# Performance work log

Hardware: AMD Instinct MI355X
Metric: run time of the kernel (lower is better)

The kernel has to match this reference:

```python
import jax, jax.numpy as jnp
import numpy as np

D = 512; H = 8; DH = 64; DI = H * DH   # dim, heads, dim_head, attn inner dim
L = 6                                   # num_blocks
NEX = 6                                 # num_message_exchanges
FFI = int(D * 4.0 * 2 / 3)              # 1365, GEGLU inner dim
V = 32000                               # num_tokens (vocab)
B, N = 2, 192                           # batch, seq_len
EPS = 1.1920929e-07                     # torch nn.RMSNorm default eps (fp32 finfo eps)


def rmsnorm(x, w):
    return x * jax.lax.rsqrt(jnp.mean(x * x, axis=-1, keepdims=True) + EPS) * w


def _heads(t):
    return t.reshape(t.shape[:-1] + (H, DH))


def _block_attn(x, nw, qw, kvw, ow):
    # x: [L, b, n, D]; per-block weights have leading L (vmap over blocks)
    h = rmsnorm(x, nw[:, None, None, :])
    q = _heads(jnp.einsum('lbnd,led->lbne', h, qw))
    kv = jnp.einsum('lbnd,lfd->lbnf', h, kvw)
    k, v = map(_heads, jnp.split(kv, 2, axis=-1))
    sim = jnp.einsum('lbihd,lbjhd->lbhij', q, k)  # NOTE: original never applies 1/sqrt(d) scale
    attn = jax.nn.softmax(sim, axis=-1)
    o = jnp.einsum('lbhij,lbjhd->lbihd', attn, v)
    o = o.reshape(o.shape[:-2] + (DI,))
    return jnp.einsum('lbne,lde->lbnd', o, ow)


def _block_ff(x, nw, kw, kb, vw, vb):
    h = rmsnorm(x, nw[:, None, None, :])
    z = jnp.einsum('lbnd,lfd->lbnf', h, kw) + kb[:, None, None, :]
    sim, gates = jnp.split(z, 2, axis=-1)
    act = sim * jax.nn.gelu(gates, approximate=False)
    return jnp.einsum('lbnf,ldf->lbnd', act, vw) + vb[:, None, None, :]


def _pooled_attn(q_in, ctx, nw, knw, qw, kvw, ow):
    # single-query cross attention; q_in: [B', n, D], ctx: [B', n, M, D]
    qn = rmsnorm(q_in, nw)
    cn = rmsnorm(ctx, nw)
    q = _heads(jnp.einsum('bnd,ed->bne', qn, qw))
    kv = jnp.einsum('bnmd,fd->bnmf', cn, kvw)
    k, v = map(_heads, jnp.split(kv, 2, axis=-1))
    k = rmsnorm(k, knw)  # key_rmsnorm=True on residual/message attention
    sim = jnp.einsum('bnhd,bnmhd->bnhm', q, k)  # unscaled, faithful
    attn = jax.nn.softmax(sim, axis=-1)
    o = jnp.einsum('bnhm,bnmhd->bnhd', attn, v).reshape(q_in.shape[:-1] + (DI,))
    return jnp.einsum('bne,de->bnd', o, ow)


def _forward(tokens, attn_norm_w, attn_q_w, attn_kv_w, attn_out_w,
             ff_norm_w, ff_keys_w, ff_keys_b, ff_vals_w, ff_vals_b,
             res_norm_w, res_keynorm_w, res_q_w, res_kv_w, res_out_w,
             query_readout, ro_norm_w, ro_w):
    b, n, _ = tokens.shape
    toks = jnp.broadcast_to(tokens[None], (L, b, n, D))
    messages = [toks]
    for i in range(NEX):
        attended = _block_attn(toks, attn_norm_w, attn_q_w, attn_kv_w, attn_out_w)
        mem = _block_ff(toks, ff_norm_w, ff_keys_w, ff_keys_b, ff_vals_w, ff_vals_b)
        messages += [attended, mem]
        if i == NEX - 1:
            continue
        packed = jnp.concatenate(messages, axis=0)  # [M, b, n, D], M = len(messages)*L
        M = packed.shape[0]
        # repeat 'm b n d -> (b l) n m d' : all messages broadcast to every block
        am = jnp.broadcast_to(jnp.transpose(packed, (1, 2, 0, 3))[:, None],
                              (b, L, n, M, D)).reshape(b * L, n, M, D)
        # queries flattened (l b)-major vs context (b l)-major -- faithful to original pairing
        qs = toks.reshape(L * b, n, D)
        pooled = _pooled_attn(qs, am, res_norm_w, res_keynorm_w, res_q_w, res_kv_w, res_out_w)
        toks = pooled.reshape(L, b, n, D)
    # rearrange messages 'm l b n d -> b n (m l) d'
    all_m = jnp.transpose(jnp.stack(messages), (2, 3, 0, 1, 4)).reshape(b, n, -1, D)
    qr = jnp.broadcast_to(query_readout, (b, n, D))
    ro = _pooled_attn(qr, all_m, res_norm_w, res_keynorm_w, res_q_w, res_kv_w, res_out_w)
    return jnp.einsum('bnd,vd->bnv', rmsnorm(ro, ro_norm_w), ro_w)


def setup_inputs() -> dict:
    key = jax.random.key(0)
    ks = jax.random.split(key, 16)
    s = 0.02
    def rn(k, shape):
        return jax.random.normal(k, shape, jnp.float32) * s
    return {
        'tokens': jax.random.normal(ks[0], (B, N, D), jnp.float32),
        'attn_norm_w': jnp.ones((L, D), jnp.float32),
        'attn_q_w': rn(ks[1], (L, DI, D)),
        'attn_kv_w': rn(ks[2], (L, 2 * DI, D)),
        'attn_out_w': rn(ks[3], (L, D, DI)),
        'ff_norm_w': jnp.ones((L, D), jnp.float32),
        'ff_keys_w': rn(ks[4], (L, 2 * FFI, D)),
        'ff_keys_b': rn(ks[5], (L, 2 * FFI)),
        'ff_vals_w': rn(ks[6], (L, D, FFI)),
        'ff_vals_b': rn(ks[7], (L, D)),
        'res_norm_w': jnp.ones((D,), jnp.float32),
        'res_keynorm_w': jnp.ones((DH,), jnp.float32),
        'res_q_w': rn(ks[8], (DI, D)),
        'res_kv_w': rn(ks[9], (2 * DI, D)),
        'res_out_w': rn(ks[10], (D, DI)),
        'query_readout': rn(ks[11], (D,)) * 0.5,  # randn * 0.01 as in original init
        'ro_norm_w': jnp.ones((D,), jnp.float32),
        'ro_w': rn(ks[12], (V, D)),
    }


def reference(tokens, attn_norm_w, attn_q_w, attn_kv_w, attn_out_w,
              ff_norm_w, ff_keys_w, ff_keys_b, ff_vals_w, ff_vals_b,
              res_norm_w, res_keynorm_w, res_q_w, res_kv_w, res_out_w,
              query_readout, ro_norm_w, ro_w):
    return _forward(tokens, attn_norm_w, attn_q_w, attn_kv_w, attn_out_w,
                    ff_norm_w, ff_keys_w, ff_keys_b, ff_vals_w, ff_vals_b,
                    res_norm_w, res_keynorm_w, res_q_w, res_kv_w, res_out_w,
                    query_readout, ro_norm_w, ro_w)
```

## Files before the change

### kernel.cpp

```cpp
#include <hip/hip_runtime.h>
#include <hip/hip_bf16.h>
#include <math.h>


#define EPSV 1.1920929e-07f
typedef __hip_bfloat16 bf16;
typedef __attribute__((ext_vector_type(4))) float f32x4;
typedef __attribute__((ext_vector_type(8))) short bf16x8;

__device__ inline void split8r(f32x4 x0, f32x4 x1, bf16x8& h8, bf16x8& l8) {
#pragma unroll
  for (int i = 0; i < 4; ++i) {
    bf16 h0 = __float2bfloat16(x0[i]);
    h8[i] = __builtin_bit_cast(short, h0);
    l8[i] = __builtin_bit_cast(short, __float2bfloat16(x0[i] - __bfloat162float(h0)));
    bf16 h1 = __float2bfloat16(x1[i]);
    h8[i + 4] = __builtin_bit_cast(short, h1);
    l8[i + 4] = __builtin_bit_cast(short, __float2bfloat16(x1[i] - __bfloat162float(h1)));
  }
}

#define BKG 32
#define LDB 40
template <int BMN, int MR>
__global__ __launch_bounds__(256) void gemm_split_t(
    const float* __restrict__ A, const float* __restrict__ W,
    const float* __restrict__ bias, float* __restrict__ C,
    int M, int N, int K, int ldc,
    long long aStr, long long wStr, long long bStr, long long cStr, int mode)
{
  int batch = blockIdx.z;
  A += (size_t)batch * aStr;
  W += (size_t)batch * wStr;
  C += (size_t)batch * cStr;
  if (bias) bias += (size_t)batch * bStr;
  int m0 = blockIdx.y * BMN, n0 = blockIdx.x * BMN;

  __shared__ short Ah[BMN * LDB], Al[BMN * LDB];
  __shared__ short Wh[BMN * LDB], Wl[BMN * LDB];

  int t = threadIdx.x;
  int wave = t >> 6, lane = t & 63;
  const int HALF = BMN / 2;
  const int NR = BMN / 64;
  int wr = wave >> 1, wc = wave & 1;
  int fr = lane & 15, fq = lane >> 4;
  int srow = t >> 2;
  int scol = (t & 3) * 8;

  f32x4 acc[MR][MR] = {};
  f32x4 pa0[NR], pa1[NR], pw0[NR], pw1[NR];

#pragma unroll
  for (int r = 0; r < NR; ++r) {
    int row = r * 64 + srow;
    const float* pa = A + (size_t)(m0 + row) * K + scol;
    const float* pw = W + (size_t)(n0 + row) * K + scol;
    pa0[r] = *(const f32x4*)pa;  pa1[r] = *(const f32x4*)(pa + 4);
    pw0[r] = *(const f32x4*)pw;  pw1[r] = *(const f32x4*)(pw + 4);
  }

  for (int k0 = 0; k0 < K; k0 += BKG) {
#pragma unroll
    for (int r = 0; r < NR; ++r) {
      int row = r * 64 + srow;
      bf16x8 h, l;
      split8r(pa0[r], pa1[r], h, l);
      *(bf16x8*)&Ah[row * LDB + scol] = h;
      *(bf16x8*)&Al[row * LDB + scol] = l;
      split8r(pw0[r], pw1[r], h, l);
      *(bf16x8*)&Wh[row * LDB + scol] = h;
      *(bf16x8*)&Wl[row * LDB + scol] = l;
    }
    if (k0 + BKG < K) {
      int kn = k0 + BKG;
#pragma unroll
      for (int r = 0; r < NR; ++r) {
        int row = r * 64 + srow;
        const float* pa = A + (size_t)(m0 + row) * K + kn + scol;
        const float* pw = W + (size_t)(n0 + row) * K + kn + scol;
        pa0[r] = *(const f32x4*)pa;  pa1[r] = *(const f32x4*)(pa + 4);
        pw0[r] = *(const f32x4*)pw;  pw1[r] = *(const f32x4*)(pw + 4);
      }
    }
    __syncthreads();
    bf16x8 ah[MR], al[MR], wh[MR], wl[MR];
#pragma unroll
    for (int m = 0; m < MR; ++m) {
      int r = (wr * HALF + m * 16 + fr) * LDB + fq * 8;
      ah[m] = *(const bf16x8*)&Ah[r];
      al[m] = *(const bf16x8*)&Al[r];
    }
#pragma unroll
    for (int n = 0; n < MR; ++n) {
      int r = (wc * HALF + n * 16 + fr) * LDB + fq * 8;
      wh[n] = *(const bf16x8*)&Wh[r];
      wl[n] = *(const bf16x8*)&Wl[r];
    }
#pragma unroll
    for (int m = 0; m < MR; ++m)
#pragma unroll
      for (int n = 0; n < MR; ++n) {
        acc[m][n] = __builtin_amdgcn_mfma_f32_16x16x32_bf16(ah[m], wh[n], acc[m][n], 0, 0, 0);
        acc[m][n] = __builtin_amdgcn_mfma_f32_16x16x32_bf16(al[m], wh[n], acc[m][n], 0, 0, 0);
        acc[m][n] = __builtin_amdgcn_mfma_f32_16x16x32_bf16(ah[m], wl[n], acc[m][n], 0, 0, 0);
      }
    __syncthreads();
  }

  if (mode == 0) {
#pragma unroll
    for (int m = 0; m < MR; ++m)
#pragma unroll
      for (int n = 0; n < MR; ++n) {
        int col = n0 + wc * HALF + n * 16 + fr;
        if (col >= N) continue;
        float bv = bias ? bias[col] : 0.f;
#pragma unroll
        for (int j = 0; j < 4; ++j) {
          int row = m0 + wr * HALF + m * 16 + fq * 4 + j;
          if (row < M) C[(size_t)row * ldc + col] = acc[m][n][j] + bv;
        }
      }
  } else {
#pragma unroll
    for (int m = 0; m < MR; ++m)
#pragma unroll
      for (int n = 0; n < MR; ++n) {
        int col = n0 + wc * HALF + n * 16 + fr;
        float bv = bias[col];
#pragma unroll
        for (int j = 0; j < 4; ++j) {
          float z = acc[m][n][j] + bv;
          float zn = __shfl_xor(z, 1);
          if (!(col & 1) && col < N) {
            float g = zn;
            float a = z * (0.5f * g * (1.f + erff(g * 0.70710678118654752f)));
            int row = m0 + wr * HALF + m * 16 + fq * 4 + j;
            if (row < M) C[(size_t)row * ldc + (col >> 1)] = a;
          }
        }
      }
  }
}

__global__ void ffk_perm_kernel(const float* __restrict__ kw,
                                const float* __restrict__ kb,
                                float* __restrict__ wout, float* __restrict__ bout)
{
  size_t idx = (size_t)blockIdx.x * 256 + threadIdx.x;
  const size_t per = 2816ull * 512;
  if (idx < 6 * per) {
    int b = (int)(idx / per);
    size_t r2 = idx % per;
    int r = (int)(r2 >> 9), k = (int)(r2 & 511);
    float v = 0.f;
    if (r < 2730) {
      int c = (r >> 1) + (r & 1) * 1365;
      v = kw[((size_t)b * 2730 + c) * 512 + k];
    }
    wout[idx] = v;
  }
  if (idx < 6 * 2816) {
    int b = (int)(idx / 2816), r = (int)(idx % 2816);
    float v = 0.f;
    if (r < 2730) {
      int c = (r >> 1) + (r & 1) * 1365;
      v = kb[(size_t)b * 2730 + c];
    }
    bout[idx] = v;
  }
}

__global__ void ffv_pad_kernel(const float* __restrict__ vw, float* __restrict__ wout)
{
  size_t idx = (size_t)blockIdx.x * 256 + threadIdx.x;
  const size_t total = 6ull * 512 * 1408;
  if (idx >= total) return;
  int k = (int)(idx % 1408);
  size_t nr = idx / 1408;
  wout[idx] = (k < 1365) ? vw[nr * 1365 + k] : 0.f;
}

__global__ __launch_bounds__(256) void rmsnorm_kernel(
    const float* __restrict__ x, const float* __restrict__ w,
    float* __restrict__ out, int rows_per_w)
{
  int r = blockIdx.x;
  int t = threadIdx.x;
  const float* xr = x + (size_t)r * 512;
  float a = xr[t], b = xr[t + 256];
  float ss = a * a + b * b;
  for (int off = 32; off; off >>= 1) ss += __shfl_xor(ss, off);
  __shared__ float wsum[4];
  if ((t & 63) == 0) wsum[t >> 6] = ss;
  __syncthreads();
  float tot = wsum[0] + wsum[1] + wsum[2] + wsum[3];
  float rs = rsqrtf(tot * (1.f / 512.f) + EPSV);
  const float* wr = w + (size_t)(r / rows_per_w) * 512;
  out[(size_t)r * 512 + t] = a * rs * wr[t];
  out[(size_t)r * 512 + t + 256] = b * rs * wr[t + 256];
}

__global__ __launch_bounds__(256) void rmsnorm2_kernel(
    const float* __restrict__ x, const float* __restrict__ w1,
    const float* __restrict__ w2, float* __restrict__ o1,
    float* __restrict__ o2, int rows_per_w)
{
  int r = blockIdx.x;
  int t = threadIdx.x;
  const float* xr = x + (size_t)r * 512;
  float a = xr[t], b = xr[t + 256];
  float ss = a * a + b * b;
  for (int off = 32; off; off >>= 1) ss += __shfl_xor(ss, off);
  __shared__ float wsum[4];
  if ((t & 63) == 0) wsum[t >> 6] = ss;
  __syncthreads();
  float tot = wsum[0] + wsum[1] + wsum[2] + wsum[3];
  float rs = rsqrtf(tot * (1.f / 512.f) + EPSV);
  int wrow = r / rows_per_w;
  float ar = a * rs, br = b * rs;
  o1[(size_t)r * 512 + t]       = ar * w1[(size_t)wrow * 512 + t];
  o1[(size_t)r * 512 + t + 256] = br * w1[(size_t)wrow * 512 + t + 256];
  o2[(size_t)r * 512 + t]       = ar * w2[(size_t)wrow * 512 + t];
  o2[(size_t)r * 512 + t + 256] = br * w2[(size_t)wrow * 512 + t + 256];
}

__global__ void bcast_kernel(const float* __restrict__ tokens, float* __restrict__ toks)
{
  size_t idx = (size_t)blockIdx.x * 256 + threadIdx.x;
  const size_t total = (size_t)6 * 2 * 192 * 512;
  if (idx >= total) return;
  toks[idx] = tokens[idx % ((size_t)2 * 192 * 512)];
}

__global__ __launch_bounds__(512) void block_attn_kernel(
    const float* __restrict__ q, const float* __restrict__ kv, float* __restrict__ o)
{
  int h = blockIdx.y, lb = blockIdx.z;
  int t = threadIdx.x;
  int wave = t >> 6, lane = t & 63;
  int i = blockIdx.x * 8 + wave;

  __shared__ float Ks[192][65];
  __shared__ float qs[8][64];
  __shared__ float ps[8][192];

  const float* kb = kv + (size_t)lb * 192 * 1024 + h * 64;
#pragma unroll
  for (int c = 0; c < 24; ++c) {
    int idx = c * 512 + t;
    int row = idx >> 6, col = idx & 63;
    Ks[row][col] = kb[(size_t)row * 1024 + col];
  }
  const float* qrow = q + ((size_t)(lb * 192 + i)) * 512 + h * 64;
  qs[wave][lane] = qrow[lane];
  __syncthreads();

  float s[3];
#pragma unroll
  for (int r = 0; r < 3; ++r) {
    int j = lane + r * 64;
    float acc = 0.f;
#pragma unroll 8
    for (int d = 0; d < 64; ++d) acc += qs[wave][d] * Ks[j][d];
    s[r] = acc;
  }
  float mx = fmaxf(fmaxf(s[0], s[1]), s[2]);
  for (int off = 32; off; off >>= 1) mx = fmaxf(mx, __shfl_xor(mx, off));
  float sum = 0.f;
#pragma unroll
  for (int r = 0; r < 3; ++r) { s[r] = expf(s[r] - mx); sum += s[r]; }
  for (int off = 32; off; off >>= 1) sum += __shfl_xor(sum, off);
  float inv = 1.f / sum;
#pragma unroll
  for (int r = 0; r < 3; ++r) ps[wave][lane + r * 64] = s[r] * inv;

  __syncthreads();
  const float* vb = kb + 512;
#pragma unroll
  for (int c = 0; c < 24; ++c) {
    int idx = c * 512 + t;
    int row = idx >> 6, col = idx & 63;
    Ks[row][col] = vb[(size_t)row * 1024 + col];
  }
  __syncthreads();
  float acc = 0.f;
  for (int j = 0; j < 192; ++j) acc += ps[wave][j] * Ks[j][lane];
  o[((size_t)(lb * 192 + i)) * 512 + h * 64 + lane] = acc;
}

__global__ __launch_bounds__(64) void pooled_attn_kernel(
    const float* __restrict__ q, const float* __restrict__ Kc,
    const float* __restrict__ Vc, float* __restrict__ o, int M, int mode)
{
  int n = blockIdx.x, h = blockIdx.y, z = blockIdx.z;
  int lane = threadIdx.x;
  int nq = mode ? 1 : 6;

  __shared__ float Ks[80][65];
  __shared__ float qs[6][64];
  __shared__ float p[6][128];

  for (int m = 0; m < M; ++m)
    Ks[m][lane] = Kc[(((size_t)m * 2 + z) * 192 + n) * 512 + h * 64 + lane];
  for (int jj = 0; jj < nq; ++jj) {
    const float* qrow = mode ? (q + h * 64)
                             : (q + ((size_t)((z * 6 + jj) * 192 + n)) * 512 + h * 64);
    qs[jj][lane] = qrow[lane];
  }
  __syncthreads();

  float d0[6] = {}, d1[6] = {};
  int m1 = lane + 64;
#pragma unroll 4
  for (int d = 0; d < 64; ++d) {
    float k0 = Ks[lane][d];
    float k1 = Ks[m1 & 79][d];
#pragma unroll
    for (int jj = 0; jj < 6; ++jj) {
      float qv = qs[jj][d];
      d0[jj] += qv * k0;
      d1[jj] += qv * k1;
    }
  }
  float acc[6] = {};
#pragma unroll
  for (int jj = 0; jj < 6; ++jj) {
    if (jj >= nq) break;
    float s0 = (lane < M) ? d0[jj] : -1e30f;
    float s1 = (m1 < M) ? d1[jj] : -1e30f;
    float mx = fmaxf(s0, s1);
    for (int off = 32; off; off >>= 1) mx = fmaxf(mx, __shfl_xor(mx, off));
    float e0 = (lane < M) ? expf(s0 - mx) : 0.f;
    float e1 = (m1 < M) ? expf(s1 - mx) : 0.f;
    float sum = e0 + e1;
    for (int off = 32; off; off >>= 1) sum += __shfl_xor(sum, off);
    float inv = 1.f / sum;
    p[jj][lane] = e0 * inv;
    p[jj][m1] = e1 * inv;
  }
  __syncthreads();

  for (int m = 0; m < M; ++m) {
    float v = Vc[(((size_t)m * 2 + z) * 192 + n) * 512 + h * 64 + lane];
#pragma unroll
    for (int jj = 0; jj < 6; ++jj) acc[jj] += p[jj][m] * v;
  }
#pragma unroll
  for (int jj = 0; jj < 6; ++jj) {
    if (jj >= nq) break;
    int orow = mode ? (z * 192 + n) : ((z * 6 + jj) * 192 + n);
    o[(size_t)orow * 512 + h * 64 + lane] = acc[jj];
  }
}

__global__ __launch_bounds__(128) void cache_fill_kernel(
    const float* __restrict__ kvp, const float* __restrict__ knw,
    float* __restrict__ Kc, float* __restrict__ Vc, int base_e)
{
  int n = blockIdx.x;
  int t = blockIdx.y;
  int g = t >> 1, b = t & 1;
  int e = base_e + g;
  int lane = threadIdx.x;
  const float* src = kvp + ((size_t)t * 192 + n) * 1024;
  float k4[4];
  float ss = 0.f;
#pragma unroll
  for (int u = 0; u < 4; ++u) { k4[u] = src[lane * 4 + u]; ss += k4[u] * k4[u]; }
  for (int off = 8; off; off >>= 1) ss += __shfl_xor(ss, off, 16);
  float rs = rsqrtf(ss * (1.f / 64.f) + EPSV);
  float* kd = Kc + (((size_t)e * 2 + b) * 192 + n) * 512;
  float* vd = Vc + (((size_t)e * 2 + b) * 192 + n) * 512;
#pragma unroll
  for (int u = 0; u < 4; ++u) {
    int c = lane * 4 + u;
    kd[c] = k4[u] * rs * knw[c & 63];
    vd[c] = src[512 + c];
  }
}

extern "C" void kernel_launch(void* const* d_in, const int* in_sizes, int n_in,
                              void* d_out, int out_size, void* d_ws, size_t ws_size,
                              hipStream_t stream)
{
  const float* tokens   = (const float*)d_in[0];
  const float* attn_nw  = (const float*)d_in[1];
  const float* attn_qw  = (const float*)d_in[2];
  const float* attn_kvw = (const float*)d_in[3];
  const float* attn_ow  = (const float*)d_in[4];
  const float* ff_nw    = (const float*)d_in[5];
  const float* ff_kw    = (const float*)d_in[6];
  const float* ff_kb    = (const float*)d_in[7];
  const float* ff_vw    = (const float*)d_in[8];
  const float* ff_vb    = (const float*)d_in[9];
  const float* res_nw   = (const float*)d_in[10];
  const float* res_knw  = (const float*)d_in[11];
  const float* res_qw   = (const float*)d_in[12];
  const float* res_kvw  = (const float*)d_in[13];
  const float* res_ow   = (const float*)d_in[14];
  const float* q_ro     = (const float*)d_in[15];
  const float* ro_nw    = (const float*)d_in[16];
  const float* ro_w     = (const float*)d_in[17];
  float* out = (float*)d_out;

  float* ws = (float*)d_ws;
  const size_t NEED = 54281728ull * 4ull;
  if (ws_size < NEED) return;
  float* ffk_w   = ws;  ws += 6ull * 2816 * 512;
  float* ffk_b   = ws;  ws += 6ull * 2816;
  float* ffv_w   = ws;  ws += 6ull * 512 * 1408;
  float* toks    = ws;  ws += 1179648;
  float* hbuf    = ws;  ws += 2359296;
  float* msgbuf  = ws;  ws += 2359296;
  float* scratch = ws;  ws += 4718592;
  float* rqn     = ws;  ws += 512;
  float* rq      = ws;  ws += 512;
  float* Kc      = ws;  ws += 15335424;
  float* Vc      = ws;  ws += 15335424;
  float* qbuf   = scratch;
  float* kvbuf  = scratch + 1179648;
  float* obuf   = scratch + 3538944;
  float* kvpool = scratch;
  float* act    = scratch;
  float* hbuf2  = hbuf + 1179648;
  float* robuf  = msgbuf;
  float* robuf2 = msgbuf + 196608;
  float* ronorm = msgbuf + 393216;

  auto gemm = [&](const float* A, const float* W, const float* bias, float* C,
                  int M, int N, int K, int ldc,
                  long long aStr, long long wStr, long long bStr, long long cStr,
                  int nb, int mode) {
    int gx = (N + 127) / 128, gy = (M + 127) / 128;
    if (mode == 0 && gx * gy * nb <= 144) {
      dim3 g((N + 63) / 64, (M + 63) / 64, nb);
      hipLaunchKernelGGL((gemm_split_t<64, 2>), g, dim3(256), 0, stream,
                         A, W, bias, C, M, N, K, ldc, aStr, wStr, bStr, cStr, mode);
    } else {
      dim3 g(gx, gy, nb);
      hipLaunchKernelGGL((gemm_split_t<128, 4>), g, dim3(256), 0, stream,
                         A, W, bias, C, M, N, K, ldc, aStr, wStr, bStr, cStr, mode);
    }
  };

  hipLaunchKernelGGL(ffk_perm_kernel, dim3((unsigned)((6ull * 2816 * 512 + 255) / 256)),
                     dim3(256), 0, stream, ff_kw, ff_kb, ffk_w, ffk_b);
  hipLaunchKernelGGL(ffv_pad_kernel, dim3((unsigned)((6ull * 512 * 1408 + 255) / 256)),
                     dim3(256), 0, stream, ff_vw, ffv_w);

  {
    const int total = 6 * 2 * 192 * 512;
    hipLaunchKernelGGL(bcast_kernel, dim3((total + 255) / 256), dim3(256), 0, stream,
                       tokens, toks);
  }
  hipLaunchKernelGGL(rmsnorm_kernel, dim3(2304), dim3(256), 0, stream,
                     toks, res_nw, hbuf, 2304);
  gemm(hbuf, res_kvw, nullptr, kvpool, 384, 1024, 512, 1024,
       196608, 0, 0, 393216, 6, 0);
  hipLaunchKernelGGL(cache_fill_kernel, dim3(192, 12), dim3(128), 0, stream,
                     kvpool, res_knw, Kc, Vc, 0);

  for (int it = 0; it < 6; ++it) {
    hipLaunchKernelGGL(rmsnorm2_kernel, dim3(2304), dim3(256), 0, stream,
                       toks, attn_nw, ff_nw, hbuf, hbuf2, 384);
    gemm(hbuf, attn_qw, nullptr, qbuf, 384, 512, 512, 512,
         196608, 262144, 0, 196608, 6, 0);
    gemm(hbuf, attn_kvw, nullptr, kvbuf, 384, 1024, 512, 1024,
         196608, 524288, 0, 393216, 6, 0);
    hipLaunchKernelGGL(block_attn_kernel, dim3(24, 8, 12), dim3(512), 0, stream,
                       qbuf, kvbuf, obuf);
    gemm(obuf, attn_ow, nullptr, msgbuf, 384, 512, 512, 512,
         196608, 262144, 0, 196608, 6, 0);
    gemm(hbuf2, ffk_w, ffk_b, act, 384, 2730, 512, 1408,
         196608, 1441792, 2816, 540672, 6, 1);
    gemm(act, ffv_w, ff_vb, msgbuf + 1179648, 384, 512, 1408, 512,
         540672, 720896, 512, 196608, 6, 0);
    hipLaunchKernelGGL(rmsnorm_kernel, dim3(4608), dim3(256), 0, stream,
                       msgbuf, res_nw, hbuf, 4608);
    gemm(hbuf, res_kvw, nullptr, kvpool, 384, 1024, 512, 1024,
         196608, 0, 0, 393216, 12, 0);
    hipLaunchKernelGGL(cache_fill_kernel, dim3(192, 24), dim3(128), 0, stream,
                       kvpool, res_knw, Kc, Vc, (2 * it + 1) * 6);
    if (it == 5) break;
    hipLaunchKernelGGL(rmsnorm_kernel, dim3(2304), dim3(256), 0, stream,
                       toks, res_nw, hbuf, 2304);
    gemm(hbuf, res_qw, nullptr, qbuf, 2304, 512, 512, 512,
         0, 0, 0, 0, 1, 0);
    hipLaunchKernelGGL(pooled_attn_kernel, dim3(192, 8, 2), dim3(64), 0, stream,
                       qbuf, Kc, Vc, obuf, (3 + 2 * it) * 6, 0);
    gemm(obuf, res_ow, nullptr, toks, 2304, 512, 512, 512,
         0, 0, 0, 0, 1, 0);
  }

  hipLaunchKernelGGL(rmsnorm_kernel, dim3(1), dim3(256), 0, stream,
                     q_ro, res_nw, rqn, 1);
  gemm(rqn, res_qw, nullptr, rq, 1, 512, 512, 512, 0, 0, 0, 0, 1, 0);
  hipLaunchKernelGGL(pooled_attn_kernel, dim3(192, 8, 2), dim3(64), 0, stream,
                     rq, Kc, Vc, robuf, 78, 1);
  gemm(robuf, res_ow, nullptr, robuf2, 384, 512, 512, 512, 0, 0, 0, 0, 1, 0);
  hipLaunchKernelGGL(rmsnorm_kernel, dim3(384), dim3(256), 0, stream,
                     robuf2, ro_nw, ronorm, 384);
  gemm(ronorm, ro_w, nullptr, out, 384, 32000, 512, 32000, 0, 0, 0, 0, 1, 0);
}
```

Baseline: 1.882 ms.

## Double-buffer GEMM global prefetch and process two queries per wave in block attention

The GEMM mainloop now keeps two stages of register-prefetched global tiles, loading two K-steps ahead so global load latency has more time to hide behind the MFMA work. The block attention kernel now handles two query rows per wave, halving the grid and reusing each K/V load from shared memory across both queries, which halves the redundant K/V staging into shared memory. The cost is higher register pressure in the GEMM and in the attention kernel, and fewer attention blocks for the GPU to schedule.

```diff
diff --git a/kernel.cpp b/kernel.cpp
--- a/kernel.cpp
+++ b/kernel.cpp
@@ -49,38 +49,46 @@
   int scol = (t & 3) * 8;
 
   f32x4 acc[MR][MR] = {};
-  f32x4 pa0[NR], pa1[NR], pw0[NR], pw1[NR];
-
-#pragma unroll
-  for (int r = 0; r < NR; ++r) {
-    int row = r * 64 + srow;
-    const float* pa = A + (size_t)(m0 + row) * K + scol;
-    const float* pw = W + (size_t)(n0 + row) * K + scol;
-    pa0[r] = *(const f32x4*)pa;  pa1[r] = *(const f32x4*)(pa + 4);
-    pw0[r] = *(const f32x4*)pw;  pw1[r] = *(const f32x4*)(pw + 4);
-  }
-
-  for (int k0 = 0; k0 < K; k0 += BKG) {
+  f32x4 pa0[2][NR], pa1[2][NR], pw0[2][NR], pw1[2][NR];
+
+  const int nsteps = K / BKG;
+#pragma unroll
+  for (int s = 0; s < 2; ++s) {
+    if (s < nsteps) {
+      int kk = s * BKG;
+#pragma unroll
+      for (int r = 0; r < NR; ++r) {
+        int row = r * 64 + srow;
+        const float* pa = A + (size_t)(m0 + row) * K + kk + scol;
+        const float* pw = W + (size_t)(n0 + row) * K + kk + scol;
+        pa0[s][r] = *(const f32x4*)pa;  pa1[s][r] = *(const f32x4*)(pa + 4);
+        pw0[s][r] = *(const f32x4*)pw;  pw1[s][r] = *(const f32x4*)(pw + 4);
+      }
+    }
+  }
+
+  for (int step = 0; step < nsteps; ++step) {
+    int cur = step & 1;
 #pragma unroll
     for (int r = 0; r < NR; ++r) {
       int row = r * 64 + srow;
       bf16x8 h, l;
-      split8r(pa0[r], pa1[r], h, l);
+      split8r(pa0[cur][r], pa1[cur][r], h, l);
       *(bf16x8*)&Ah[row * LDB + scol] = h;
       *(bf16x8*)&Al[row * LDB + scol] = l;
-      split8r(pw0[r], pw1[r], h, l);
+      split8r(pw0[cur][r], pw1[cur][r], h, l);
       *(bf16x8*)&Wh[row * LDB + scol] = h;
       *(bf16x8*)&Wl[row * LDB + scol] = l;
     }
-    if (k0 + BKG < K) {
-      int kn = k0 + BKG;
+    if (step + 2 < nsteps) {
+      int kn = (step + 2) * BKG;
 #pragma unroll
       for (int r = 0; r < NR; ++r) {
         int row = r * 64 + srow;
         const float* pa = A + (size_t)(m0 + row) * K + kn + scol;
         const float* pw = W + (size_t)(n0 + row) * K + kn + scol;
-        pa0[r] = *(const f32x4*)pa;  pa1[r] = *(const f32x4*)(pa + 4);
-        pw0[r] = *(const f32x4*)pw;  pw1[r] = *(const f32x4*)(pw + 4);
+        pa0[cur][r] = *(const f32x4*)pa;  pa1[cur][r] = *(const f32x4*)(pa + 4);
+        pw0[cur][r] = *(const f32x4*)pw;  pw1[cur][r] = *(const f32x4*)(pw + 4);
       }
     }
     __syncthreads();
@@ -240,11 +248,11 @@
   int h = blockIdx.y, lb = blockIdx.z;
   int t = threadIdx.x;
   int wave = t >> 6, lane = t & 63;
-  int i = blockIdx.x * 8 + wave;
+  int i0 = blockIdx.x * 16 + wave * 2;
 
   __shared__ float Ks[192][65];
-  __shared__ float qs[8][64];
-  __shared__ float ps[8][192];
+  __shared__ float qs[8][2][64];
+  __shared__ float ps[16][192];
 
   const float* kb = kv + (size_t)lb * 192 * 1024 + h * 64;
 #pragma unroll
@@ -253,28 +261,37 @@
     int row = idx >> 6, col = idx & 63;
     Ks[row][col] = kb[(size_t)row * 1024 + col];
   }
-  const float* qrow = q + ((size_t)(lb * 192 + i)) * 512 + h * 64;
-  qs[wave][lane] = qrow[lane];
-  __syncthreads();
-
-  float s[3];
+#pragma unroll
+  for (int qq = 0; qq < 2; ++qq)
+    qs[wave][qq][lane] = q[((size_t)(lb * 192 + i0 + qq)) * 512 + h * 64 + lane];
+  __syncthreads();
+
+  float s[2][3];
 #pragma unroll
   for (int r = 0; r < 3; ++r) {
     int j = lane + r * 64;
-    float acc = 0.f;
+    float a0 = 0.f, a1 = 0.f;
 #pragma unroll 8
-    for (int d = 0; d < 64; ++d) acc += qs[wave][d] * Ks[j][d];
-    s[r] = acc;
-  }
-  float mx = fmaxf(fmaxf(s[0], s[1]), s[2]);
-  for (int off = 32; off; off >>= 1) mx = fmaxf(mx, __shfl_xor(mx, off));
-  float sum = 0.f;
-#pragma unroll
-  for (int r = 0; r < 3; ++r) { s[r] = expf(s[r] - mx); sum += s[r]; }
-  for (int off = 32; off; off >>= 1) sum += __shfl_xor(sum, off);
-  float inv = 1.f / sum;
-#pragma unroll
-  for (int r = 0; r < 3; ++r) ps[wave][lane + r * 64] = s[r] * inv;
+    for (int d = 0; d < 64; ++d) {
+      float kvl = Ks[j][d];
+      a0 += qs[wave][0][d] * kvl;
+      a1 += qs[wave][1][d] * kvl;
+    }
+    s[0][r] = a0;
+    s[1][r] = a1;
+  }
+#pragma unroll
+  for (int qq = 0; qq < 2; ++qq) {
+    float mx = fmaxf(fmaxf(s[qq][0], s[qq][1]), s[qq][2]);
+    for (int off = 32; off; off >>= 1) mx = fmaxf(mx, __shfl_xor(mx, off));
+    float sum = 0.f;
+#pragma unroll
+    for (int r = 0; r < 3; ++r) { s[qq][r] = expf(s[qq][r] - mx); sum += s[qq][r]; }
+    for (int off = 32; off; off >>= 1) sum += __shfl_xor(sum, off);
+    float inv = 1.f / sum;
+#pragma unroll
+    for (int r = 0; r < 3; ++r) ps[wave * 2 + qq][lane + r * 64] = s[qq][r] * inv;
+  }
 
   __syncthreads();
   const float* vb = kb + 512;
@@ -285,9 +302,14 @@
     Ks[row][col] = vb[(size_t)row * 1024 + col];
   }
   __syncthreads();
-  float acc = 0.f;
-  for (int j = 0; j < 192; ++j) acc += ps[wave][j] * Ks[j][lane];
-  o[((size_t)(lb * 192 + i)) * 512 + h * 64 + lane] = acc;
+  float acc0 = 0.f, acc1 = 0.f;
+  for (int j = 0; j < 192; ++j) {
+    float v = Ks[j][lane];
+    acc0 += ps[wave * 2][j] * v;
+    acc1 += ps[wave * 2 + 1][j] * v;
+  }
+  o[((size_t)(lb * 192 + i0)) * 512 + h * 64 + lane] = acc0;
+  o[((size_t)(lb * 192 + i0 + 1)) * 512 + h * 64 + lane] = acc1;
 }
 
 __global__ __launch_bounds__(64) void pooled_attn_kernel(
@@ -469,7 +491,7 @@
          196608, 262144, 0, 196608, 6, 0);
     gemm(hbuf, attn_kvw, nullptr, kvbuf, 384, 1024, 512, 1024,
          196608, 524288, 0, 393216, 6, 0);
-    hipLaunchKernelGGL(block_attn_kernel, dim3(24, 8, 12), dim3(512), 0, stream,
+    hipLaunchKernelGGL(block_attn_kernel, dim3(12, 8, 12), dim3(512), 0, stream,
                        qbuf, kvbuf, obuf);
     gemm(obuf, attn_ow, nullptr, msgbuf, 384, 512, 512, 512,
          196608, 262144, 0, 196608, 6, 0);
```

Result: slower. 2.767 ms (+47.0%).
